# Kernel optimization log

Hardware: AMD Instinct MI355X
Metric: run time of the kernel (lower is better)

The kernel has to match this reference:

```python
import jax, jax.numpy as jnp
import numpy as np

N_NODES = 100000
N_EDGES = 3200000
FEAT = 128
HID = 128
N_GRAPHS = 512


def setup_inputs() -> dict:
    key = jax.random.key(0)
    ks = jax.random.split(key, 16)
    x = jax.random.normal(ks[0], (N_NODES, FEAT), dtype=jnp.float32)
    edge_index = jax.random.randint(ks[1], (2, N_EDGES), 0, N_NODES, dtype=jnp.int32)
    edge_weight = jax.random.uniform(ks[2], (N_EDGES,), dtype=jnp.float32)
    batch = jnp.sort(jax.random.randint(ks[3], (N_NODES,), 0, N_GRAPHS, dtype=jnp.int32))
    s = 1.0 / np.sqrt(HID)
    W1 = jax.random.uniform(ks[4], (FEAT, HID), dtype=jnp.float32, minval=-s, maxval=s)
    W2 = jax.random.uniform(ks[5], (HID, HID), dtype=jnp.float32, minval=-s, maxval=s)
    W3 = jax.random.uniform(ks[6], (HID, HID), dtype=jnp.float32, minval=-s, maxval=s)
    W4 = jax.random.uniform(ks[7], (HID, HID), dtype=jnp.float32, minval=-s, maxval=s)
    b1 = jnp.zeros((HID,), jnp.float32)
    b2 = jnp.zeros((HID,), jnp.float32)
    b3 = jnp.zeros((HID,), jnp.float32)
    b4 = jnp.zeros((HID,), jnp.float32)
    Wc = jax.random.uniform(ks[8], (HID, 1), dtype=jnp.float32, minval=-s, maxval=s)
    bc = jnp.zeros((1,), jnp.float32)
    return dict(x=x, edge_index=edge_index, edge_weight=edge_weight, batch=batch,
                W1=W1, b1=b1, W2=W2, b2=b2, W3=W3, b3=b3, W4=W4, b4=b4, Wc=Wc, bc=bc)


def _gcn_norm(edge_index, edge_weight, n):
    # PyG gcn_norm with add_self_loops=True (self-loop weight 1)
    loop = jnp.arange(n, dtype=edge_index.dtype)
    src = jnp.concatenate([edge_index[0], loop])
    dst = jnp.concatenate([edge_index[1], loop])
    ew = jnp.concatenate([edge_weight, jnp.ones((n,), edge_weight.dtype)])
    deg = jax.ops.segment_sum(ew, dst, num_segments=n)
    dinv = jnp.where(deg > 0, jax.lax.rsqrt(jnp.maximum(deg, 1e-30)), 0.0)
    norm = dinv[src] * ew * dinv[dst]
    return src, dst, norm


def _gcn_conv(x, src, dst, norm, W, b, n):
    h = x @ W                      # [N, H] dense GEMM
    msg = h[src] * norm[:, None]   # [E+N, H] gather + scale
    out = jax.ops.segment_sum(msg, dst, num_segments=n)  # scatter-add
    return out + b


def reference(x, edge_index, edge_weight, batch,
              W1, b1, W2, b2, W3, b3, W4, b4, Wc, bc):
    n = x.shape[0]
    src, dst, norm = _gcn_norm(edge_index, edge_weight, n)
    h = jax.nn.relu(_gcn_conv(x, src, dst, norm, W1, b1, n))
    h = jax.nn.relu(_gcn_conv(h, src, dst, norm, W2, b2, n))
    h = jax.nn.relu(_gcn_conv(h, src, dst, norm, W3, b3, n))
    h = jax.nn.relu(_gcn_conv(h, src, dst, norm, W4, b4, n))
    # global mean pool over graphs
    sums = jax.ops.segment_sum(h, batch, num_segments=N_GRAPHS)
    cnt = jax.ops.segment_sum(jnp.ones((n,), h.dtype), batch, num_segments=N_GRAPHS)
    pooled = sums / jnp.maximum(cnt, 1.0)[:, None]
    return jax.nn.sigmoid(pooled @ Wc + bc)
```

## Files before the change

kernel.cpp:

```cpp
#include <hip/hip_runtime.h>
#include <math.h>


#define MASK40 ((1ull << 40) - 1)

typedef float v2f __attribute__((ext_vector_type(2)));
typedef __bf16 bf16x8 __attribute__((ext_vector_type(8)));
typedef float f32x4 __attribute__((ext_vector_type(4)));

__device__ inline unsigned f2bf(float x) {
    unsigned u = __float_as_uint(x);
    return (u + 0x7FFFu + ((u >> 16) & 1u)) >> 16;
}

__global__ void edge_pass(const int* __restrict__ dst, const float* __restrict__ ew,
                          unsigned long long* packed, unsigned short* __restrict__ slot,
                          int E) {
    int e = blockIdx.x * blockDim.x + threadIdx.x;
    if (e < E) {
        int d = dst[e];
        unsigned int fx = (unsigned int)rintf(ew[e] * 16777216.0f);
        unsigned long long old =
            atomicAdd(&packed[d], (1ull << 40) | (unsigned long long)fx);
        slot[e] = (unsigned short)(old >> 40);
    }
}

__global__ __launch_bounds__(1024) void scan1(const unsigned long long* __restrict__ packed,
                                              float* __restrict__ dinv, int* rowp,
                                              int* bsums, int total, int N) {
    __shared__ int sh[1024];
    int i = blockIdx.x * 1024 + threadIdx.x;
    int v = 0;
    if (i < N) {
        unsigned long long p = packed[i];
        float deg = 1.0f + (float)(p & MASK40) * (1.0f / 16777216.0f);
        dinv[i] = rsqrtf(deg);
        v = (int)(p >> 40) + 1;
    }
    sh[threadIdx.x] = v;
    __syncthreads();
    for (int off = 1; off < 1024; off <<= 1) {
        int t = (threadIdx.x >= (unsigned)off) ? sh[threadIdx.x - off] : 0;
        __syncthreads();
        sh[threadIdx.x] += t;
        __syncthreads();
    }
    if (i < total) rowp[i] = sh[threadIdx.x] - v;
    if (threadIdx.x == 1023) bsums[blockIdx.x] = sh[1023];
}

__global__ void scan2(int* bsums, int nb) {
    if (threadIdx.x == 0 && blockIdx.x == 0) {
        int run = 0;
        for (int b = 0; b < nb; ++b) { int t = bsums[b]; bsums[b] = run; run += t; }
    }
}

__global__ __launch_bounds__(1024) void scan3(int* rowp, const int* __restrict__ bsums,
                                              int total) {
    int i = blockIdx.x * 1024 + threadIdx.x;
    if (i < total) rowp[i] += bsums[blockIdx.x];
}

__global__ void selfloop_k(const int* __restrict__ rowp, const float* __restrict__ dinv,
                           int2* colval, int n) {
    int i = blockIdx.x * blockDim.x + threadIdx.x;
    if (i < n) {
        float dv = dinv[i];
        int2 cv;
        cv.x = i;
        cv.y = __float_as_int(dv * dv);
        colval[rowp[i]] = cv;
    }
}

__global__ void scatter2(const int* __restrict__ src, const int* __restrict__ dst,
                         const float* __restrict__ ew,
                         const unsigned short* __restrict__ slot,
                         const float* __restrict__ dinv, const int* __restrict__ rowp,
                         int2* colval, int E) {
    int e = blockIdx.x * blockDim.x + threadIdx.x;
    if (e < E) {
        int s = src[e], d = dst[e];
        int idx = rowp[d] + 1 + (int)slot[e];
        int2 cv;
        cv.x = s;
        cv.y = __float_as_int(dinv[s] * ew[e] * dinv[d]);
        colval[idx] = cv;
    }
}

__global__ void prep_w(const float* __restrict__ Wa, const float* __restrict__ Wb,
                       const float* __restrict__ Wc, const float* __restrict__ Wd,
                       unsigned short* __restrict__ Wt) {
    const int l = blockIdx.y;
    const float* W = (l == 0) ? Wa : (l == 1) ? Wb : (l == 2) ? Wc : Wd;
    const int c = blockIdx.x, p = threadIdx.x;
    int k;
    if (l == 0) {
        k = p;
    } else {
        int t = p >> 1, h = p & 1;
        int i = t >> 2, s = (t >> 1) & 1, jj = 2 * (t & 1) + h;
        k = 16 * (4 * s + jj) + i;
    }
    float v = W[k * 128 + c];
    unsigned u = __float_as_uint(v);
    Wt[l * 16384 + c * 128 + p] = (unsigned short)((u + 0x7FFFu + ((u >> 16) & 1u)) >> 16);
}

template <int FP32IN>
__global__ __launch_bounds__(256) void gemm_mfma(const void* __restrict__ Av,
                                                 const uint4* __restrict__ Wt,
                                                 uint2* __restrict__ C, int N) {
    const int w = threadIdx.x >> 6;
    const int lane = threadIdx.x & 63;
    const int li = lane & 15, q = lane >> 4;
    const long row_base = (long)blockIdx.x * 64 + w * 16;
    const long arow = (row_base + li < (long)N) ? row_base + li : (long)N - 1;

    f32x4 acc[8];
#pragma unroll
    for (int t = 0; t < 8; ++t) acc[t] = (f32x4){0.f, 0.f, 0.f, 0.f};

#pragma unroll
    for (int ks = 0; ks < 4; ++ks) {
        bf16x8 af;
        if (FP32IN) {
            const float* Ar = (const float*)Av + arow * 128 + ks * 32 + q * 8;
            const float4 fa = *(const float4*)Ar;
            const float4 fb = *(const float4*)(Ar + 4);
            uint4 u;
            u.x = f2bf(fa.x) | (f2bf(fa.y) << 16);
            u.y = f2bf(fa.z) | (f2bf(fa.w) << 16);
            u.z = f2bf(fb.x) | (f2bf(fb.y) << 16);
            u.w = f2bf(fb.z) | (f2bf(fb.w) << 16);
            af = __builtin_bit_cast(bf16x8, u);
        } else {
            af = __builtin_bit_cast(bf16x8,
                ((const uint4*)Av)[arow * 16 + ks * 4 + q]);
        }
#pragma unroll
        for (int ct = 0; ct < 8; ++ct) {
            const bf16x8 bf = __builtin_bit_cast(
                bf16x8, Wt[(size_t)(ct * 16 + li) * 16 + ks * 4 + q]);
            acc[ct] = __builtin_amdgcn_mfma_f32_16x16x32_bf16(af, bf, acc[ct], 0, 0, 0);
        }
    }

#pragma unroll
    for (int reg = 0; reg < 4; ++reg) {
        int d0 = __builtin_amdgcn_cvt_pk_fp8_f32(acc[0][reg], acc[1][reg], 0, false);
        d0     = __builtin_amdgcn_cvt_pk_fp8_f32(acc[2][reg], acc[3][reg], d0, true);
        int d1 = __builtin_amdgcn_cvt_pk_fp8_f32(acc[4][reg], acc[5][reg], 0, false);
        d1     = __builtin_amdgcn_cvt_pk_fp8_f32(acc[6][reg], acc[7][reg], d1, true);
        const long row = row_base + q * 4 + reg;
        uint2 o; o.x = (unsigned)d0; o.y = (unsigned)d1;
        C[row * 16 + li] = o;
    }
}

__global__ __launch_bounds__(64) void aggregate2(const unsigned* __restrict__ t32,
                                                 const int* __restrict__ rowp,
                                                 const int2* __restrict__ colval,
                                                 const float* __restrict__ bias,
                                                 unsigned* __restrict__ out16, int n) {
    const int v0 = blockIdx.x * 2;
    const int lane = threadIdx.x;
    const int h = lane >> 5, il = lane & 31;

    const int base0 = rowp[v0];
    const int mid   = rowp[v0 + 1];
    const bool have1 = (v0 + 1) < n;
    const int end1  = have1 ? rowp[v0 + 2] : mid;
    const int len0 = mid - base0;
    const int len1 = end1 - mid;
    const int maxlen = (len0 > len1) ? len0 : len1;
    const int lenh = h ? len1 : len0;

    float a0 = 0.f, a1 = 0.f, a2 = 0.f, a3 = 0.f;
    int j = 0;
    for (; j + 4 <= maxlen; j += 4) {
#pragma unroll
        for (int k = 0; k < 4; ++k) {
            const int jj = j + k;
            const int j0 = (jj < len0) ? jj : len0 - 1;
            const int j1 = (jj < len1) ? jj : len1 - 1;
            const int2 ca = colval[base0 + j0];
            const int2 cb = colval[mid + j1];
            const int c = h ? cb.x : ca.x;
            float w = __int_as_float(h ? cb.y : ca.y);
            w = (jj < lenh) ? w : 0.f;
            const unsigned u = t32[(size_t)c * 32 + il];
            const v2f lo = __builtin_amdgcn_cvt_pk_f32_fp8((int)u, false);
            const v2f hi = __builtin_amdgcn_cvt_pk_f32_fp8((int)u, true);
            a0 = fmaf(w, lo.x, a0); a1 = fmaf(w, lo.y, a1);
            a2 = fmaf(w, hi.x, a2); a3 = fmaf(w, hi.y, a3);
        }
    }
    for (; j < maxlen; ++j) {
        const int j0 = (j < len0) ? j : len0 - 1;
        const int j1 = (j < len1) ? j : len1 - 1;
        const int2 ca = colval[base0 + j0];
        const int2 cb = colval[mid + j1];
        const int c = h ? cb.x : ca.x;
        float w = __int_as_float(h ? cb.y : ca.y);
        w = (j < lenh) ? w : 0.f;
        const unsigned u = t32[(size_t)c * 32 + il];
        const v2f lo = __builtin_amdgcn_cvt_pk_f32_fp8((int)u, false);
        const v2f hi = __builtin_amdgcn_cvt_pk_f32_fp8((int)u, true);
        a0 = fmaf(w, lo.x, a0); a1 = fmaf(w, lo.y, a1);
        a2 = fmaf(w, hi.x, a2); a3 = fmaf(w, hi.y, a3);
    }

    const int f0 = 64 * (il & 1) + (il >> 1);
    const float r0 = fmaxf(a0 + bias[f0],      0.f);
    const float r1 = fmaxf(a1 + bias[f0 + 16], 0.f);
    const float r2 = fmaxf(a2 + bias[f0 + 32], 0.f);
    const float r3 = fmaxf(a3 + bias[f0 + 48], 0.f);
    const int v = v0 + h;
    if (v < n) {
        uint2 o;
        o.x = f2bf(r0) | (f2bf(r1) << 16);
        o.y = f2bf(r2) | (f2bf(r3) << 16);
        *(uint2*)&out16[(size_t)v * 64 + il * 2] = o;
    }
}

__global__ __launch_bounds__(64) void aggregate2_last(const unsigned* __restrict__ t32,
                                                      const int* __restrict__ rowp,
                                                      const int2* __restrict__ colval,
                                                      const float* __restrict__ bias,
                                                      const float* __restrict__ Wc,
                                                      float* __restrict__ sv, int n) {
    const int v0 = blockIdx.x * 2;
    const int lane = threadIdx.x;
    const int h = lane >> 5, il = lane & 31;

    const int base0 = rowp[v0];
    const int mid   = rowp[v0 + 1];
    const bool have1 = (v0 + 1) < n;
    const int end1  = have1 ? rowp[v0 + 2] : mid;
    const int len0 = mid - base0;
    const int len1 = end1 - mid;
    const int maxlen = (len0 > len1) ? len0 : len1;
    const int lenh = h ? len1 : len0;

    float a0 = 0.f, a1 = 0.f, a2 = 0.f, a3 = 0.f;
    int j = 0;
    for (; j + 4 <= maxlen; j += 4) {
#pragma unroll
        for (int k = 0; k < 4; ++k) {
            const int jj = j + k;
            const int j0 = (jj < len0) ? jj : len0 - 1;
            const int j1 = (jj < len1) ? jj : len1 - 1;
            const int2 ca = colval[base0 + j0];
            const int2 cb = colval[mid + j1];
            const int c = h ? cb.x : ca.x;
            float w = __int_as_float(h ? cb.y : ca.y);
            w = (jj < lenh) ? w : 0.f;
            const unsigned u = t32[(size_t)c * 32 + il];
            const v2f lo = __builtin_amdgcn_cvt_pk_f32_fp8((int)u, false);
            const v2f hi = __builtin_amdgcn_cvt_pk_f32_fp8((int)u, true);
            a0 = fmaf(w, lo.x, a0); a1 = fmaf(w, lo.y, a1);
            a2 = fmaf(w, hi.x, a2); a3 = fmaf(w, hi.y, a3);
        }
    }
    for (; j < maxlen; ++j) {
        const int j0 = (j < len0) ? j : len0 - 1;
        const int j1 = (j < len1) ? j : len1 - 1;
        const int2 ca = colval[base0 + j0];
        const int2 cb = colval[mid + j1];
        const int c = h ? cb.x : ca.x;
        float w = __int_as_float(h ? cb.y : ca.y);
        w = (j < lenh) ? w : 0.f;
        const unsigned u = t32[(size_t)c * 32 + il];
        const v2f lo = __builtin_amdgcn_cvt_pk_f32_fp8((int)u, false);
        const v2f hi = __builtin_amdgcn_cvt_pk_f32_fp8((int)u, true);
        a0 = fmaf(w, lo.x, a0); a1 = fmaf(w, lo.y, a1);
        a2 = fmaf(w, hi.x, a2); a3 = fmaf(w, hi.y, a3);
    }

    const int f0 = 64 * (il & 1) + (il >> 1);
    float p = fmaxf(a0 + bias[f0],      0.f) * Wc[f0]
            + fmaxf(a1 + bias[f0 + 16], 0.f) * Wc[f0 + 16]
            + fmaxf(a2 + bias[f0 + 32], 0.f) * Wc[f0 + 32]
            + fmaxf(a3 + bias[f0 + 48], 0.f) * Wc[f0 + 48];
#pragma unroll
    for (int off = 16; off; off >>= 1) p += __shfl_xor(p, off);
    const int v = v0 + h;
    if (il == 0 && v < n) sv[v] = p;
}

__global__ void gstart_k(const int* __restrict__ batch, int* start, int N, int G) {
    int g = blockIdx.x * blockDim.x + threadIdx.x;
    if (g <= G) {
        int lo = 0, hi = N;
        while (lo < hi) {
            int mid = (lo + hi) >> 1;
            if (batch[mid] < g) lo = mid + 1; else hi = mid;
        }
        start[g] = lo;
    }
}

__global__ __launch_bounds__(256) void seg_pool(const float* __restrict__ sv,
                                                const int* __restrict__ start,
                                                const float* __restrict__ bc,
                                                float* __restrict__ out, int G) {
    __shared__ float sh[4];
    const int g = blockIdx.x;
    const int s = start[g], epos = start[g + 1];
    float acc = 0.f;
    for (int i = s + threadIdx.x; i < epos; i += 256) acc += sv[i];
#pragma unroll
    for (int off = 32; off; off >>= 1) acc += __shfl_down(acc, off);
    if ((threadIdx.x & 63) == 0) sh[threadIdx.x >> 6] = acc;
    __syncthreads();
    if (threadIdx.x == 0) {
        float sum = sh[0] + sh[1] + sh[2] + sh[3];
        float cnt = (float)(epos - s);
        float z = sum / fmaxf(cnt, 1.0f) + bc[0];
        out[g] = 1.0f / (1.0f + expf(-z));
    }
}

extern "C" void kernel_launch(void* const* d_in, const int* in_sizes, int n_in,
                              void* d_out, int out_size, void* d_ws, size_t ws_size,
                              hipStream_t stream) {
    const float* x   = (const float*)d_in[0];
    const int* ei    = (const int*)d_in[1];
    const float* ew  = (const float*)d_in[2];
    const int* batch = (const int*)d_in[3];
    const float* W1 = (const float*)d_in[4];  const float* b1 = (const float*)d_in[5];
    const float* W2 = (const float*)d_in[6];  const float* b2 = (const float*)d_in[7];
    const float* W3 = (const float*)d_in[8];  const float* b3 = (const float*)d_in[9];
    const float* W4 = (const float*)d_in[10]; const float* b4 = (const float*)d_in[11];
    const float* Wc = (const float*)d_in[12]; const float* bc = (const float*)d_in[13];

    const int N = in_sizes[0] / 128;
    const int E = in_sizes[2];
    const int G = out_size;
    const int* src = ei;
    const int* dst = ei + E;
    const int nblk = (N + 63) / 64;
    const long Npad = (long)nblk * 64;

    char* p = (char*)d_ws;
    auto alloc = [&](size_t bytes) {
        void* q = (void*)p;
        p += (bytes + 255) & ~(size_t)255;
        return q;
    };
    unsigned long long* packed = (unsigned long long*)alloc((size_t)N * 8);
    float* dinv = (float*)alloc((size_t)N * 4);
    unsigned short* slot = (unsigned short*)alloc((size_t)E * 2);
    int* rowp   = (int*)alloc((size_t)(N + 1) * 4);
    int* bsums  = (int*)alloc(1024 * 4);
    const size_t M = (size_t)E + (size_t)N;
    int2* colval = (int2*)alloc(M * 8);
    unsigned* tbuf = (unsigned*)alloc((size_t)Npad * 32 * 4);
    unsigned* hbuf = (unsigned*)alloc((size_t)Npad * 64 * 4);
    unsigned short* Wt = (unsigned short*)alloc(4 * 16384 * 2);
    float* sv   = (float*)alloc((size_t)N * 4);
    int* start  = (int*)alloc((size_t)(G + 1) * 4);

    const int B = 256;
    hipMemsetAsync(packed, 0, (size_t)N * 8, stream);
    edge_pass<<<(E + B - 1) / B, B, 0, stream>>>(dst, ew, packed, slot, E);
    const int total = N + 1;
    const int nb = (total + 1023) / 1024;
    scan1<<<nb, 1024, 0, stream>>>(packed, dinv, rowp, bsums, total, N);
    scan2<<<1, 64, 0, stream>>>(bsums, nb);
    scan3<<<nb, 1024, 0, stream>>>(rowp, bsums, total);
    selfloop_k<<<(N + B - 1) / B, B, 0, stream>>>(rowp, dinv, colval, N);
    scatter2<<<(E + B - 1) / B, B, 0, stream>>>(src, dst, ew, slot, dinv, rowp,
                                                colval, E);
    gstart_k<<<(G + 1 + B - 1) / B, B, 0, stream>>>(batch, start, N, G);
    prep_w<<<dim3(128, 4), 128, 0, stream>>>(W1, W2, W3, W4, Wt);

    const int agrid = (N + 1) / 2;
    const uint4* Wt4 = (const uint4*)Wt;
    gemm_mfma<1><<<nblk, B, 0, stream>>>(x,    Wt4,        (uint2*)tbuf, N);
    aggregate2<<<agrid, 64, 0, stream>>>(tbuf, rowp, colval, b1, hbuf, N);
    gemm_mfma<0><<<nblk, B, 0, stream>>>(hbuf, Wt4 + 2048, (uint2*)tbuf, N);
    aggregate2<<<agrid, 64, 0, stream>>>(tbuf, rowp, colval, b2, hbuf, N);
    gemm_mfma<0><<<nblk, B, 0, stream>>>(hbuf, Wt4 + 4096, (uint2*)tbuf, N);
    aggregate2<<<agrid, 64, 0, stream>>>(tbuf, rowp, colval, b3, hbuf, N);
    gemm_mfma<0><<<nblk, B, 0, stream>>>(hbuf, Wt4 + 6144, (uint2*)tbuf, N);
    aggregate2_last<<<agrid, 64, 0, stream>>>(tbuf, rowp, colval, b4, Wc, sv, N);

    seg_pool<<<G, B, 0, stream>>>(sv, start, bc, (float*)d_out, G);
}
```

Baseline: 816.7 us.

## Merge edge counting, first GEMM and graph-start search into one launch; widen aggregate blocks

```diff
diff --git a/kernel.cpp b/kernel.cpp
--- a/kernel.cpp
+++ b/kernel.cpp
@@ -13,111 +13,15 @@
     return (u + 0x7FFFu + ((u >> 16) & 1u)) >> 16;
 }
 
-__global__ void edge_pass(const int* __restrict__ dst, const float* __restrict__ ew,
-                          unsigned long long* packed, unsigned short* __restrict__ slot,
-                          int E) {
-    int e = blockIdx.x * blockDim.x + threadIdx.x;
-    if (e < E) {
-        int d = dst[e];
-        unsigned int fx = (unsigned int)rintf(ew[e] * 16777216.0f);
-        unsigned long long old =
-            atomicAdd(&packed[d], (1ull << 40) | (unsigned long long)fx);
-        slot[e] = (unsigned short)(old >> 40);
-    }
-}
-
-__global__ __launch_bounds__(1024) void scan1(const unsigned long long* __restrict__ packed,
-                                              float* __restrict__ dinv, int* rowp,
-                                              int* bsums, int total, int N) {
-    __shared__ int sh[1024];
-    int i = blockIdx.x * 1024 + threadIdx.x;
-    int v = 0;
-    if (i < N) {
-        unsigned long long p = packed[i];
-        float deg = 1.0f + (float)(p & MASK40) * (1.0f / 16777216.0f);
-        dinv[i] = rsqrtf(deg);
-        v = (int)(p >> 40) + 1;
-    }
-    sh[threadIdx.x] = v;
-    __syncthreads();
-    for (int off = 1; off < 1024; off <<= 1) {
-        int t = (threadIdx.x >= (unsigned)off) ? sh[threadIdx.x - off] : 0;
-        __syncthreads();
-        sh[threadIdx.x] += t;
-        __syncthreads();
-    }
-    if (i < total) rowp[i] = sh[threadIdx.x] - v;
-    if (threadIdx.x == 1023) bsums[blockIdx.x] = sh[1023];
-}
-
-__global__ void scan2(int* bsums, int nb) {
-    if (threadIdx.x == 0 && blockIdx.x == 0) {
-        int run = 0;
-        for (int b = 0; b < nb; ++b) { int t = bsums[b]; bsums[b] = run; run += t; }
-    }
-}
-
-__global__ __launch_bounds__(1024) void scan3(int* rowp, const int* __restrict__ bsums,
-                                              int total) {
-    int i = blockIdx.x * 1024 + threadIdx.x;
-    if (i < total) rowp[i] += bsums[blockIdx.x];
-}
-
-__global__ void selfloop_k(const int* __restrict__ rowp, const float* __restrict__ dinv,
-                           int2* colval, int n) {
-    int i = blockIdx.x * blockDim.x + threadIdx.x;
-    if (i < n) {
-        float dv = dinv[i];
-        int2 cv;
-        cv.x = i;
-        cv.y = __float_as_int(dv * dv);
-        colval[rowp[i]] = cv;
-    }
-}
-
-__global__ void scatter2(const int* __restrict__ src, const int* __restrict__ dst,
-                         const float* __restrict__ ew,
-                         const unsigned short* __restrict__ slot,
-                         const float* __restrict__ dinv, const int* __restrict__ rowp,
-                         int2* colval, int E) {
-    int e = blockIdx.x * blockDim.x + threadIdx.x;
-    if (e < E) {
-        int s = src[e], d = dst[e];
-        int idx = rowp[d] + 1 + (int)slot[e];
-        int2 cv;
-        cv.x = s;
-        cv.y = __float_as_int(dinv[s] * ew[e] * dinv[d]);
-        colval[idx] = cv;
-    }
-}
-
-__global__ void prep_w(const float* __restrict__ Wa, const float* __restrict__ Wb,
-                       const float* __restrict__ Wc, const float* __restrict__ Wd,
-                       unsigned short* __restrict__ Wt) {
-    const int l = blockIdx.y;
-    const float* W = (l == 0) ? Wa : (l == 1) ? Wb : (l == 2) ? Wc : Wd;
-    const int c = blockIdx.x, p = threadIdx.x;
-    int k;
-    if (l == 0) {
-        k = p;
-    } else {
-        int t = p >> 1, h = p & 1;
-        int i = t >> 2, s = (t >> 1) & 1, jj = 2 * (t & 1) + h;
-        k = 16 * (4 * s + jj) + i;
-    }
-    float v = W[k * 128 + c];
-    unsigned u = __float_as_uint(v);
-    Wt[l * 16384 + c * 128 + p] = (unsigned short)((u + 0x7FFFu + ((u >> 16) & 1u)) >> 16);
-}
-
 template <int FP32IN>
-__global__ __launch_bounds__(256) void gemm_mfma(const void* __restrict__ Av,
-                                                 const uint4* __restrict__ Wt,
-                                                 uint2* __restrict__ C, int N) {
-    const int w = threadIdx.x >> 6;
-    const int lane = threadIdx.x & 63;
+__device__ __forceinline__ void gemm_body(const void* __restrict__ Av,
+                                          const uint4* __restrict__ Wt,
+                                          uint2* __restrict__ C, int N,
+                                          int bid, int tid) {
+    const int w = tid >> 6;
+    const int lane = tid & 63;
     const int li = lane & 15, q = lane >> 4;
-    const long row_base = (long)blockIdx.x * 64 + w * 16;
+    const long row_base = (long)bid * 64 + w * 16;
     const long arow = (row_base + li < (long)N) ? row_base + li : (long)N - 1;
 
     f32x4 acc[8];
@@ -161,13 +65,139 @@
     }
 }
 
-__global__ __launch_bounds__(64) void aggregate2(const unsigned* __restrict__ t32,
-                                                 const int* __restrict__ rowp,
-                                                 const int2* __restrict__ colval,
-                                                 const float* __restrict__ bias,
-                                                 unsigned* __restrict__ out16, int n) {
-    const int v0 = blockIdx.x * 2;
-    const int lane = threadIdx.x;
+__global__ __launch_bounds__(256) void gemm_mfma_k(const void* __restrict__ Av,
+                                                   const uint4* __restrict__ Wt,
+                                                   uint2* __restrict__ C, int N) {
+    gemm_body<0>(Av, Wt, C, N, blockIdx.x, threadIdx.x);
+}
+
+__global__ __launch_bounds__(256) void front_k(const int* __restrict__ dst,
+                                               const float* __restrict__ ew,
+                                               unsigned long long* packed,
+                                               unsigned short* __restrict__ slot,
+                                               int E, int nE,
+                                               const float* __restrict__ x,
+                                               const uint4* __restrict__ Wt,
+                                               uint2* __restrict__ tbuf, int N, int nG,
+                                               const int* __restrict__ batch,
+                                               int* start, int G) {
+    const int b = blockIdx.x;
+    if (b < nE) {
+        int e = b * 256 + threadIdx.x;
+        if (e < E) {
+            int d = dst[e];
+            unsigned int fx = (unsigned int)rintf(ew[e] * 16777216.0f);
+            unsigned long long old =
+                atomicAdd(&packed[d], (1ull << 40) | (unsigned long long)fx);
+            slot[e] = (unsigned short)(old >> 40);
+        }
+    } else if (b < nE + nG) {
+        gemm_body<1>(x, Wt, tbuf, N, b - nE, threadIdx.x);
+    } else {
+        int g = (b - nE - nG) * 256 + threadIdx.x;
+        if (g <= G) {
+            int lo = 0, hi = N;
+            while (lo < hi) {
+                int mid = (lo + hi) >> 1;
+                if (batch[mid] < g) lo = mid + 1; else hi = mid;
+            }
+            start[g] = lo;
+        }
+    }
+}
+
+__global__ __launch_bounds__(1024) void scan1(const unsigned long long* __restrict__ packed,
+                                              float* __restrict__ dinv, int* rowp,
+                                              int* bsums, int total, int N) {
+    __shared__ int sh[1024];
+    int i = blockIdx.x * 1024 + threadIdx.x;
+    int v = 0;
+    if (i < N) {
+        unsigned long long p = packed[i];
+        float deg = 1.0f + (float)(p & MASK40) * (1.0f / 16777216.0f);
+        dinv[i] = rsqrtf(deg);
+        v = (int)(p >> 40) + 1;
+    }
+    sh[threadIdx.x] = v;
+    __syncthreads();
+    for (int off = 1; off < 1024; off <<= 1) {
+        int t = (threadIdx.x >= (unsigned)off) ? sh[threadIdx.x - off] : 0;
+        __syncthreads();
+        sh[threadIdx.x] += t;
+        __syncthreads();
+    }
+    if (i < total) rowp[i] = sh[threadIdx.x] - v;
+    if (threadIdx.x == 1023) bsums[blockIdx.x] = sh[1023];
+}
+
+__global__ void scan2(int* bsums, int nb) {
+    if (threadIdx.x == 0 && blockIdx.x == 0) {
+        int run = 0;
+        for (int b = 0; b < nb; ++b) { int t = bsums[b]; bsums[b] = run; run += t; }
+    }
+}
+
+__global__ __launch_bounds__(1024) void scan3(int* rowp, const int* __restrict__ bsums,
+                                              int total) {
+    int i = blockIdx.x * 1024 + threadIdx.x;
+    if (i < total) rowp[i] += bsums[blockIdx.x];
+}
+
+__global__ void selfloop_k(const int* __restrict__ rowp, const float* __restrict__ dinv,
+                           int2* colval, int n) {
+    int i = blockIdx.x * blockDim.x + threadIdx.x;
+    if (i < n) {
+        float dv = dinv[i];
+        int2 cv;
+        cv.x = i;
+        cv.y = __float_as_int(dv * dv);
+        colval[rowp[i]] = cv;
+    }
+}
+
+__global__ void scatter2(const int* __restrict__ src, const int* __restrict__ dst,
+                         const float* __restrict__ ew,
+                         const unsigned short* __restrict__ slot,
+                         const float* __restrict__ dinv, const int* __restrict__ rowp,
+                         int2* colval, int E) {
+    int e = blockIdx.x * blockDim.x + threadIdx.x;
+    if (e < E) {
+        int s = src[e], d = dst[e];
+        int idx = rowp[d] + 1 + (int)slot[e];
+        int2 cv;
+        cv.x = s;
+        cv.y = __float_as_int(dinv[s] * ew[e] * dinv[d]);
+        colval[idx] = cv;
+    }
+}
+
+__global__ void prep_w(const float* __restrict__ Wa, const float* __restrict__ Wb,
+                       const float* __restrict__ Wc, const float* __restrict__ Wd,
+                       unsigned short* __restrict__ Wt) {
+    const int l = blockIdx.y;
+    const float* W = (l == 0) ? Wa : (l == 1) ? Wb : (l == 2) ? Wc : Wd;
+    const int c = blockIdx.x, p = threadIdx.x;
+    int k;
+    if (l == 0) {
+        k = p;
+    } else {
+        int t = p >> 1, h = p & 1;
+        int i = t >> 2, s = (t >> 1) & 1, jj = 2 * (t & 1) + h;
+        k = 16 * (4 * s + jj) + i;
+    }
+    float v = W[k * 128 + c];
+    unsigned u = __float_as_uint(v);
+    Wt[l * 16384 + c * 128 + p] = (unsigned short)((u + 0x7FFFu + ((u >> 16) & 1u)) >> 16);
+}
+
+__global__ __launch_bounds__(256) void aggregate2(const unsigned* __restrict__ t32,
+                                                  const int* __restrict__ rowp,
+                                                  const int2* __restrict__ colval,
+                                                  const float* __restrict__ bias,
+                                                  unsigned* __restrict__ out16, int n) {
+    const int v0 = blockIdx.x * 8 + ((threadIdx.x >> 6) << 1);
+    if (v0 >= n) return;
+    const int lane = threadIdx.x & 63;
     const int h = lane >> 5, il = lane & 31;
 
     const int base0 = rowp[v0];
@@ -228,14 +258,15 @@
     }
 }
 
-__global__ __launch_bounds__(64) void aggregate2_last(const unsigned* __restrict__ t32,
-                                                      const int* __restrict__ rowp,
-                                                      const int2* __restrict__ colval,
-                                                      const float* __restrict__ bias,
-                                                      const float* __restrict__ Wc,
-                                                      float* __restrict__ sv, int n) {
-    const int v0 = blockIdx.x * 2;
-    const int lane = threadIdx.x;
+__global__ __launch_bounds__(256) void aggregate2_last(const unsigned* __restrict__ t32,
+                                                       const int* __restrict__ rowp,
+                                                       const int2* __restrict__ colval,
+                                                       const float* __restrict__ bias,
+                                                       const float* __restrict__ Wc,
+                                                       float* __restrict__ sv, int n) {
+    const int v0 = blockIdx.x * 8 + ((threadIdx.x >> 6) << 1);
+    if (v0 >= n) return;
+    const int lane = threadIdx.x & 63;
     const int h = lane >> 5, il = lane & 31;
 
     const int base0 = rowp[v0];
@@ -291,18 +322,6 @@
     for (int off = 16; off; off >>= 1) p += __shfl_xor(p, off);
     const int v = v0 + h;
     if (il == 0 && v < n) sv[v] = p;
-}
-
-__global__ void gstart_k(const int* __restrict__ batch, int* start, int N, int G) {
-    int g = blockIdx.x * blockDim.x + threadIdx.x;
-    if (g <= G) {
-        int lo = 0, hi = N;
-        while (lo < hi) {
-            int mid = (lo + hi) >> 1;
-            if (batch[mid] < g) lo = mid + 1; else hi = mid;
-        }
-        start[g] = lo;
-    }
 }
 
 __global__ __launch_bounds__(256) void seg_pool(const float* __restrict__ sv,
@@ -367,8 +386,17 @@
     int* start  = (int*)alloc((size_t)(G + 1) * 4);
 
     const int B = 256;
+    const uint4* Wt4 = (const uint4*)Wt;
+
     hipMemsetAsync(packed, 0, (size_t)N * 8, stream);
-    edge_pass<<<(E + B - 1) / B, B, 0, stream>>>(dst, ew, packed, slot, E);
+    prep_w<<<dim3(128, 4), 128, 0, stream>>>(W1, W2, W3, W4, Wt);
+
+    const int nE = (E + B - 1) / B;
+    const int gb = (G + 1 + B - 1) / B;
+    front_k<<<nE + nblk + gb, B, 0, stream>>>(dst, ew, packed, slot, E, nE,
+                                              x, Wt4, (uint2*)tbuf, N, nblk,
+                                              batch, start, G);
+
     const int total = N + 1;
     const int nb = (total + 1023) / 1024;
     scan1<<<nb, 1024, 0, stream>>>(packed, dinv, rowp, bsums, total, N);
@@ -377,19 +405,15 @@
     selfloop_k<<<(N + B - 1) / B, B, 0, stream>>>(rowp, dinv, colval, N);
     scatter2<<<(E + B - 1) / B, B, 0, stream>>>(src, dst, ew, slot, dinv, rowp,
                                                 colval, E);
-    gstart_k<<<(G + 1 + B - 1) / B, B, 0, stream>>>(batch, start, N, G);
-    prep_w<<<dim3(128, 4), 128, 0, stream>>>(W1, W2, W3, W4, Wt);
-
-    const int agrid = (N + 1) / 2;
-    const uint4* Wt4 = (const uint4*)Wt;
-    gemm_mfma<1><<<nblk, B, 0, stream>>>(x,    Wt4,        (uint2*)tbuf, N);
-    aggregate2<<<agrid, 64, 0, stream>>>(tbuf, rowp, colval, b1, hbuf, N);
-    gemm_mfma<0><<<nblk, B, 0, stream>>>(hbuf, Wt4 + 2048, (uint2*)tbuf, N);
-    aggregate2<<<agrid, 64, 0, stream>>>(tbuf, rowp, colval, b2, hbuf, N);
-    gemm_mfma<0><<<nblk, B, 0, stream>>>(hbuf, Wt4 + 4096, (uint2*)tbuf, N);
-    aggregate2<<<agrid, 64, 0, stream>>>(tbuf, rowp, colval, b3, hbuf, N);
-    gemm_mfma<0><<<nblk, B, 0, stream>>>(hbuf, Wt4 + 6144, (uint2*)tbuf, N);
-    aggregate2_last<<<agrid, 64, 0, stream>>>(tbuf, rowp, colval, b4, Wc, sv, N);
+
+    const int agrid = (N + 7) / 8;
+    aggregate2<<<agrid, B, 0, stream>>>(tbuf, rowp, colval, b1, hbuf, N);
+    gemm_mfma_k<<<nblk, B, 0, stream>>>(hbuf, Wt4 + 2048, (uint2*)tbuf, N);
+    aggregate2<<<agrid, B, 0, stream>>>(tbuf, rowp, colval, b2, hbuf, N);
+    gemm_mfma_k<<<nblk, B, 0, stream>>>(hbuf, Wt4 + 4096, (uint2*)tbuf, N);
+    aggregate2<<<agrid, B, 0, stream>>>(tbuf, rowp, colval, b3, hbuf, N);
+    gemm_mfma_k<<<nblk, B, 0, stream>>>(hbuf, Wt4 + 6144, (uint2*)tbuf, N);
+    aggregate2_last<<<agrid, B, 0, stream>>>(tbuf, rowp, colval, b4, Wc, sv, N);
 
     seg_pool<<<G, B, 0, stream>>>(sv, start, bc, (float*)d_out, G);
 }
```

Measured after the change: 1.010 ms. 1.24x slower.

## Quantize transformed features to int4 with per-row scales for aggregation

Applied to the files above, without the earlier changes.

```diff
diff --git a/kernel.cpp b/kernel.cpp
--- a/kernel.cpp
+++ b/kernel.cpp
@@ -4,13 +4,17 @@
 
 #define MASK40 ((1ull << 40) - 1)
 
-typedef float v2f __attribute__((ext_vector_type(2)));
 typedef __bf16 bf16x8 __attribute__((ext_vector_type(8)));
 typedef float f32x4 __attribute__((ext_vector_type(4)));
 
 __device__ inline unsigned f2bf(float x) {
     unsigned u = __float_as_uint(x);
     return (u + 0x7FFFu + ((u >> 16) & 1u)) >> 16;
+}
+
+__device__ inline float dec4(unsigned u, int k) {
+    int v = ((int)(u << (28 - 4 * k))) >> 28;
+    return (float)v;
 }
 
 __global__ void edge_pass(const int* __restrict__ dst, const float* __restrict__ ew,
@@ -91,6 +95,18 @@
     }
 }
 
+__global__ void gstart_k(const int* __restrict__ batch, int* start, int N, int G) {
+    int g = blockIdx.x * blockDim.x + threadIdx.x;
+    if (g <= G) {
+        int lo = 0, hi = N;
+        while (lo < hi) {
+            int mid = (lo + hi) >> 1;
+            if (batch[mid] < g) lo = mid + 1; else hi = mid;
+        }
+        start[g] = lo;
+    }
+}
+
 __global__ void prep_w(const float* __restrict__ Wa, const float* __restrict__ Wb,
                        const float* __restrict__ Wc, const float* __restrict__ Wd,
                        unsigned short* __restrict__ Wt) {
@@ -113,7 +129,8 @@
 template <int FP32IN>
 __global__ __launch_bounds__(256) void gemm_mfma(const void* __restrict__ Av,
                                                  const uint4* __restrict__ Wt,
-                                                 uint2* __restrict__ C, int N) {
+                                                 unsigned* __restrict__ C4,
+                                                 float* __restrict__ sc, int N) {
     const int w = threadIdx.x >> 6;
     const int lane = threadIdx.x & 63;
     const int li = lane & 15, q = lane >> 4;
@@ -151,17 +168,26 @@
 
 #pragma unroll
     for (int reg = 0; reg < 4; ++reg) {
-        int d0 = __builtin_amdgcn_cvt_pk_fp8_f32(acc[0][reg], acc[1][reg], 0, false);
-        d0     = __builtin_amdgcn_cvt_pk_fp8_f32(acc[2][reg], acc[3][reg], d0, true);
-        int d1 = __builtin_amdgcn_cvt_pk_fp8_f32(acc[4][reg], acc[5][reg], 0, false);
-        d1     = __builtin_amdgcn_cvt_pk_fp8_f32(acc[6][reg], acc[7][reg], d1, true);
+        float amax = 0.f;
+#pragma unroll
+        for (int ct = 0; ct < 8; ++ct) amax = fmaxf(amax, fabsf(acc[ct][reg]));
+#pragma unroll
+        for (int m = 1; m < 16; m <<= 1) amax = fmaxf(amax, __shfl_xor(amax, m));
+        const float qs = (amax > 0.f) ? 7.0f / amax : 0.f;
         const long row = row_base + q * 4 + reg;
-        uint2 o; o.x = (unsigned)d0; o.y = (unsigned)d1;
-        C[row * 16 + li] = o;
-    }
-}
-
-__global__ __launch_bounds__(64) void aggregate2(const unsigned* __restrict__ t32,
+        if (li == 0) sc[row] = amax * (1.0f / 7.0f);
+        unsigned u = 0;
+#pragma unroll
+        for (int ct = 0; ct < 8; ++ct) {
+            const int v = (int)rintf(acc[ct][reg] * qs);
+            u |= ((unsigned)v & 15u) << (ct * 4);
+        }
+        C4[row * 16 + li] = u;
+    }
+}
+
+__global__ __launch_bounds__(64) void aggregate2(const unsigned short* __restrict__ t16,
+                                                 const float* __restrict__ sc,
                                                  const int* __restrict__ rowp,
                                                  const int2* __restrict__ colval,
                                                  const float* __restrict__ bias,
@@ -189,14 +215,16 @@
             const int j1 = (jj < len1) ? jj : len1 - 1;
             const int2 ca = colval[base0 + j0];
             const int2 cb = colval[mid + j1];
+            const float sa = sc[ca.x];
+            const float sb = sc[cb.x];
             const int c = h ? cb.x : ca.x;
-            float w = __int_as_float(h ? cb.y : ca.y);
+            float w = __int_as_float(h ? cb.y : ca.y) * (h ? sb : sa);
             w = (jj < lenh) ? w : 0.f;
-            const unsigned u = t32[(size_t)c * 32 + il];
-            const v2f lo = __builtin_amdgcn_cvt_pk_f32_fp8((int)u, false);
-            const v2f hi = __builtin_amdgcn_cvt_pk_f32_fp8((int)u, true);
-            a0 = fmaf(w, lo.x, a0); a1 = fmaf(w, lo.y, a1);
-            a2 = fmaf(w, hi.x, a2); a3 = fmaf(w, hi.y, a3);
+            const unsigned u = t16[(size_t)c * 32 + il];
+            a0 = fmaf(w, dec4(u, 0), a0);
+            a1 = fmaf(w, dec4(u, 1), a1);
+            a2 = fmaf(w, dec4(u, 2), a2);
+            a3 = fmaf(w, dec4(u, 3), a3);
         }
     }
     for (; j < maxlen; ++j) {
@@ -204,14 +232,16 @@
         const int j1 = (j < len1) ? j : len1 - 1;
         const int2 ca = colval[base0 + j0];
         const int2 cb = colval[mid + j1];
+        const float sa = sc[ca.x];
+        const float sb = sc[cb.x];
         const int c = h ? cb.x : ca.x;
-        float w = __int_as_float(h ? cb.y : ca.y);
+        float w = __int_as_float(h ? cb.y : ca.y) * (h ? sb : sa);
         w = (j < lenh) ? w : 0.f;
-        const unsigned u = t32[(size_t)c * 32 + il];
-        const v2f lo = __builtin_amdgcn_cvt_pk_f32_fp8((int)u, false);
-        const v2f hi = __builtin_amdgcn_cvt_pk_f32_fp8((int)u, true);
-        a0 = fmaf(w, lo.x, a0); a1 = fmaf(w, lo.y, a1);
-        a2 = fmaf(w, hi.x, a2); a3 = fmaf(w, hi.y, a3);
+        const unsigned u = t16[(size_t)c * 32 + il];
+        a0 = fmaf(w, dec4(u, 0), a0);
+        a1 = fmaf(w, dec4(u, 1), a1);
+        a2 = fmaf(w, dec4(u, 2), a2);
+        a3 = fmaf(w, dec4(u, 3), a3);
     }
 
     const int f0 = 64 * (il & 1) + (il >> 1);
@@ -228,7 +258,8 @@
     }
 }
 
-__global__ __launch_bounds__(64) void aggregate2_last(const unsigned* __restrict__ t32,
+__global__ __launch_bounds__(64) void aggregate2_last(const unsigned short* __restrict__ t16,
+                                                      const float* __restrict__ sc,
                                                       const int* __restrict__ rowp,
                                                       const int2* __restrict__ colval,
                                                       const float* __restrict__ bias,
@@ -257,14 +288,16 @@
             const int j1 = (jj < len1) ? jj : len1 - 1;
             const int2 ca = colval[base0 + j0];
             const int2 cb = colval[mid + j1];
+            const float sa = sc[ca.x];
+            const float sb = sc[cb.x];
             const int c = h ? cb.x : ca.x;
-            float w = __int_as_float(h ? cb.y : ca.y);
+            float w = __int_as_float(h ? cb.y : ca.y) * (h ? sb : sa);
             w = (jj < lenh) ? w : 0.f;
-            const unsigned u = t32[(size_t)c * 32 + il];
-            const v2f lo = __builtin_amdgcn_cvt_pk_f32_fp8((int)u, false);
-            const v2f hi = __builtin_amdgcn_cvt_pk_f32_fp8((int)u, true);
-            a0 = fmaf(w, lo.x, a0); a1 = fmaf(w, lo.y, a1);
-            a2 = fmaf(w, hi.x, a2); a3 = fmaf(w, hi.y, a3);
+            const unsigned u = t16[(size_t)c * 32 + il];
+            a0 = fmaf(w, dec4(u, 0), a0);
+            a1 = fmaf(w, dec4(u, 1), a1);
+            a2 = fmaf(w, dec4(u, 2), a2);
+            a3 = fmaf(w, dec4(u, 3), a3);
         }
     }
     for (; j < maxlen; ++j) {
@@ -272,14 +305,16 @@
         const int j1 = (j < len1) ? j : len1 - 1;
         const int2 ca = colval[base0 + j0];
         const int2 cb = colval[mid + j1];
+        const float sa = sc[ca.x];
+        const float sb = sc[cb.x];
         const int c = h ? cb.x : ca.x;
-        float w = __int_as_float(h ? cb.y : ca.y);
+        float w = __int_as_float(h ? cb.y : ca.y) * (h ? sb : sa);
         w = (j < lenh) ? w : 0.f;
-        const unsigned u = t32[(size_t)c * 32 + il];
-        const v2f lo = __builtin_amdgcn_cvt_pk_f32_fp8((int)u, false);
-        const v2f hi = __builtin_amdgcn_cvt_pk_f32_fp8((int)u, true);
-        a0 = fmaf(w, lo.x, a0); a1 = fmaf(w, lo.y, a1);
-        a2 = fmaf(w, hi.x, a2); a3 = fmaf(w, hi.y, a3);
+        const unsigned u = t16[(size_t)c * 32 + il];
+        a0 = fmaf(w, dec4(u, 0), a0);
+        a1 = fmaf(w, dec4(u, 1), a1);
+        a2 = fmaf(w, dec4(u, 2), a2);
+        a3 = fmaf(w, dec4(u, 3), a3);
     }
 
     const int f0 = 64 * (il & 1) + (il >> 1);
@@ -291,18 +326,6 @@
     for (int off = 16; off; off >>= 1) p += __shfl_xor(p, off);
     const int v = v0 + h;
     if (il == 0 && v < n) sv[v] = p;
-}
-
-__global__ void gstart_k(const int* __restrict__ batch, int* start, int N, int G) {
-    int g = blockIdx.x * blockDim.x + threadIdx.x;
-    if (g <= G) {
-        int lo = 0, hi = N;
-        while (lo < hi) {
-            int mid = (lo + hi) >> 1;
-            if (batch[mid] < g) lo = mid + 1; else hi = mid;
-        }
-        start[g] = lo;
-    }
 }
 
 __global__ __launch_bounds__(256) void seg_pool(const float* __restrict__ sv,
@@ -360,13 +383,16 @@
     int* bsums  = (int*)alloc(1024 * 4);
     const size_t M = (size_t)E + (size_t)N;
     int2* colval = (int2*)alloc(M * 8);
-    unsigned* tbuf = (unsigned*)alloc((size_t)Npad * 32 * 4);
+    unsigned* tbuf = (unsigned*)alloc((size_t)Npad * 16 * 4);
+    float* scb     = (float*)alloc((size_t)Npad * 4);
     unsigned* hbuf = (unsigned*)alloc((size_t)Npad * 64 * 4);
     unsigned short* Wt = (unsigned short*)alloc(4 * 16384 * 2);
     float* sv   = (float*)alloc((size_t)N * 4);
     int* start  = (int*)alloc((size_t)(G + 1) * 4);
 
     const int B = 256;
+    const uint4* Wt4 = (const uint4*)Wt;
+
     hipMemsetAsync(packed, 0, (size_t)N * 8, stream);
     edge_pass<<<(E + B - 1) / B, B, 0, stream>>>(dst, ew, packed, slot, E);
     const int total = N + 1;
@@ -381,15 +407,15 @@
     prep_w<<<dim3(128, 4), 128, 0, stream>>>(W1, W2, W3, W4, Wt);
 
     const int agrid = (N + 1) / 2;
-    const uint4* Wt4 = (const uint4*)Wt;
-    gemm_mfma<1><<<nblk, B, 0, stream>>>(x,    Wt4,        (uint2*)tbuf, N);
-    aggregate2<<<agrid, 64, 0, stream>>>(tbuf, rowp, colval, b1, hbuf, N);
-    gemm_mfma<0><<<nblk, B, 0, stream>>>(hbuf, Wt4 + 2048, (uint2*)tbuf, N);
-    aggregate2<<<agrid, 64, 0, stream>>>(tbuf, rowp, colval, b2, hbuf, N);
-    gemm_mfma<0><<<nblk, B, 0, stream>>>(hbuf, Wt4 + 4096, (uint2*)tbuf, N);
-    aggregate2<<<agrid, 64, 0, stream>>>(tbuf, rowp, colval, b3, hbuf, N);
-    gemm_mfma<0><<<nblk, B, 0, stream>>>(hbuf, Wt4 + 6144, (uint2*)tbuf, N);
-    aggregate2_last<<<agrid, 64, 0, stream>>>(tbuf, rowp, colval, b4, Wc, sv, N);
+    const unsigned short* t16 = (const unsigned short*)tbuf;
+    gemm_mfma<1><<<nblk, B, 0, stream>>>(x,    Wt4,        tbuf, scb, N);
+    aggregate2<<<agrid, 64, 0, stream>>>(t16, scb, rowp, colval, b1, hbuf, N);
+    gemm_mfma<0><<<nblk, B, 0, stream>>>(hbuf, Wt4 + 2048, tbuf, scb, N);
+    aggregate2<<<agrid, 64, 0, stream>>>(t16, scb, rowp, colval, b2, hbuf, N);
+    gemm_mfma<0><<<nblk, B, 0, stream>>>(hbuf, Wt4 + 4096, tbuf, scb, N);
+    aggregate2<<<agrid, 64, 0, stream>>>(t16, scb, rowp, colval, b3, hbuf, N);
+    gemm_mfma<0><<<nblk, B, 0, stream>>>(hbuf, Wt4 + 6144, tbuf, scb, N);
+    aggregate2_last<<<agrid, 64, 0, stream>>>(t16, scb, rowp, colval, b4, Wc, sv, N);
 
     seg_pool<<<G, B, 0, stream>>>(sv, start, bc, (float*)d_out, G);
 }
```

Result: slower. 1.128 ms (+38.2%).
